# Kernel optimization log

Measured on AMD Instinct MI355X. Metric: run time of the kernel, lower is better.

The kernel has to match this reference:

```python
import jax, jax.numpy as jnp
import numpy as np

N_NODES = 50000
N_EDGES = 800000
F_IN = 128
HIDDEN = 32
HEADS = 4
F_OUT = 64
NEG_SLOPE = 0.2


def setup_inputs() -> dict:
    key = jax.random.key(0)
    ks = jax.random.split(key, 9)
    x = jax.random.normal(ks[0], (N_NODES, F_IN), dtype=jnp.float32)
    edge_index = jax.random.randint(ks[1], (2, N_EDGES), 0, N_NODES, dtype=jnp.int64)
    edge_weight = jax.random.uniform(ks[2], (N_EDGES,), dtype=jnp.float32)
    # GATConv parameters
    W = jax.random.normal(ks[3], (F_IN, HEADS * HIDDEN), dtype=jnp.float32) * (1.0 / np.sqrt(F_IN))
    a_src = jax.random.normal(ks[4], (HEADS, HIDDEN), dtype=jnp.float32) * 0.1
    a_dst = jax.random.normal(ks[5], (HEADS, HIDDEN), dtype=jnp.float32) * 0.1
    bias = jnp.zeros((HEADS * HIDDEN,), dtype=jnp.float32)
    # output linear
    W2 = jax.random.normal(ks[6], (HEADS * HIDDEN, F_OUT), dtype=jnp.float32) * (1.0 / np.sqrt(HEADS * HIDDEN))
    b2 = jnp.zeros((F_OUT,), dtype=jnp.float32)
    return {"x": x, "edge_index": edge_index, "edge_weight": edge_weight,
            "W": W, "a_src": a_src, "a_dst": a_dst, "bias": bias,
            "W2": W2, "b2": b2}


def reference(x, edge_index, edge_weight, W, a_src, a_dst, bias, W2, b2):
    src, dst = edge_index[0], edge_index[1]
    # linear transform per head: [N, H, C]
    h = (x @ W).reshape(-1, HEADS, HIDDEN)
    # per-node attention logits: [N, H]
    alpha_s = jnp.einsum('nhc,hc->nh', h, a_src)
    alpha_d = jnp.einsum('nhc,hc->nh', h, a_dst)
    # per-edge scores: [E, H]
    e = alpha_s[src] + alpha_d[dst]
    e = jnp.where(e >= 0, e, NEG_SLOPE * e)  # LeakyReLU(0.2)
    # segment softmax over destination neighborhoods
    m = jax.ops.segment_max(e, dst, num_segments=N_NODES)  # [N, H]
    ex = jnp.exp(e - m[dst])
    denom = jax.ops.segment_sum(ex, dst, num_segments=N_NODES)  # [N, H]
    alpha = ex / (denom[dst] + 1e-16)  # [E, H]
    # weighted scatter-add aggregation: [N, H, C]
    msgs = alpha[:, :, None] * h[src]
    out = jax.ops.segment_sum(msgs, dst, num_segments=N_NODES)
    out = out.reshape(-1, HEADS * HIDDEN) + bias
    out = jax.nn.elu(out)
    return out @ W2 + b2
```

## Files before the change

### kernel.cpp

```cpp
#include <hip/hip_runtime.h>

#define N_NODES 50000
#define N_EDGES 800000
#define F_IN 128
#define HH 128
#define HEADS 4
#define F_OUT 64
#define NEG_SLOPE 0.2f

#define NBIN ((N_NODES + 63) / 64)
#define XC 8
#define CAPXB 256
#define NCUR (NBIN * XC)
#define BINCAP (XC * CAPXB)

#define NODE_BLOCKS ((N_NODES + 31) / 32)
#define FILLB (N_EDGES / 256)
#define TOTAL_BLOCKS (NODE_BLOCKS + FILLB)
#define ZERO_BLOCKS ((NCUR + 255) / 256)

typedef __attribute__((ext_vector_type(8))) short short8v;
typedef __attribute__((ext_vector_type(4))) float float4v;

__device__ __forceinline__ unsigned short f2bf(float f) {
    unsigned int u = __float_as_uint(f);
    u = (u + 0x7FFFu + ((u >> 16) & 1u)) >> 16;
    return (unsigned short)u;
}
__device__ __forceinline__ float bf2f(unsigned short s) {
    return __uint_as_float((unsigned int)s << 16);
}

__global__ __launch_bounds__(256) void k_prep(
    const float* __restrict__ W, const float* __restrict__ a_src,
    const float* __restrict__ a_dst,
    unsigned short* __restrict__ Wf, unsigned short* __restrict__ Waf,
    int* __restrict__ cursor)
{
    const int b = blockIdx.x;
    const int t = threadIdx.x;

    if (b >= 9) {
        int i = (b - 9) * 256 + t;
        if (i < NCUR) cursor[i] = 0;
        return;
    }

    if (b < 8) {
        const int ks = b >> 1, nn = b & 1;
        const int w = t >> 6, lane = t & 63, l15 = lane & 15, l4 = lane >> 4;
        const int c  = w * 32 + nn * 16 + l15;
        const int kb = ks * 32 + l4 * 8;
        short8v frag;
        #pragma unroll
        for (int j = 0; j < 8; ++j)
            frag[j] = (short)f2bf(W[(size_t)(kb + j) * HH + c]);
        *(short8v*)&Wf[(size_t)((ks * 2 + nn) * 256 + t) * 8] = frag;
        return;
    }

    __shared__ float Wa[F_IN][8];
    #pragma unroll
    for (int i = 0; i < 4; ++i) {
        int idx = t * 4 + i;
        int k = idx >> 3, col = idx & 7;
        const float* av = (col < 4) ? a_src : a_dst;
        int hd = col & 3;
        float s = 0.f;
        #pragma unroll
        for (int cc = 0; cc < 32; ++cc)
            s = fmaf(W[(size_t)k * HH + hd * 32 + cc], av[hd * 32 + cc], s);
        Wa[k][col] = s;
    }
    __syncthreads();

    if (t < 64) {
        const int l15 = t & 15, l4 = t >> 4;
        #pragma unroll
        for (int ks = 0; ks < 4; ++ks) {
            short8v frag;
            #pragma unroll
            for (int j = 0; j < 8; ++j)
                frag[j] = (l15 < 8) ? (short)f2bf(Wa[ks * 32 + l4 * 8 + j][l15]) : (short)0;
            *(short8v*)&Waf[(size_t)(ks * 64 + t) * 8] = frag;
        }
    }
}

__global__ __launch_bounds__(256) void k_node_fill(
    const float* __restrict__ x,
    const unsigned short* __restrict__ Wf, const unsigned short* __restrict__ Waf,
    unsigned short* __restrict__ h_bf,
    float* __restrict__ as_out, float* __restrict__ ad_out,
    const int* __restrict__ ei, int* __restrict__ cursor, unsigned int* __restrict__ bins)
{
    __shared__ __align__(16) unsigned short xs[32][136];

    const int g = blockIdx.x;
    if (g % 3 != 0) {
        const int fidx = g - g / 3 - 1;
        if (fidx < FILLB) {
            const int vx = g & 7;
            int e = fidx * 256 + threadIdx.x;
            int S = ei[e];
            int D = ei[N_EDGES + e];
            int idx = (D >> 6) * XC + vx;
            int sl = atomicAdd(&cursor[idx], 1);
            if (sl < CAPXB)
                bins[(size_t)idx * CAPXB + sl] =
                    ((unsigned int)S << 6) | (unsigned int)(D & 63);
        }
        return;
    }

    const int tid  = threadIdx.x;
    const int base = (g / 3) * 32;

    for (int i = tid; i < 32 * 32; i += 256) {
        int r = i >> 5, c4 = i & 31;
        int n = base + r;
        float4 v = (n < N_NODES) ? *(const float4*)&x[(size_t)n * F_IN + c4 * 4]
                                 : make_float4(0.f, 0.f, 0.f, 0.f);
        ushort4 hv;
        hv.x = f2bf(v.x); hv.y = f2bf(v.y); hv.z = f2bf(v.z); hv.w = f2bf(v.w);
        *(ushort4*)&xs[r][c4 * 4] = hv;
    }
    __syncthreads();

    const int w    = tid >> 6;
    const int lane = tid & 63;
    const int l15  = lane & 15;
    const int l4   = lane >> 4;

    short8v bfrag[4][2], wafrag[4];
    #pragma unroll
    for (int ks = 0; ks < 4; ++ks) {
        bfrag[ks][0] = *(const short8v*)&Wf[(size_t)((ks * 2 + 0) * 256 + tid) * 8];
        bfrag[ks][1] = *(const short8v*)&Wf[(size_t)((ks * 2 + 1) * 256 + tid) * 8];
        wafrag[ks]   = *(const short8v*)&Waf[(size_t)(ks * 64 + lane) * 8];
    }

    float4v acc[2][2] = {};
    float4v accL[2] = {};
    #pragma unroll
    for (int ks = 0; ks < 4; ++ks) {
        short8v a0 = *(const short8v*)&xs[l15][ks * 32 + l4 * 8];
        short8v a1 = *(const short8v*)&xs[16 + l15][ks * 32 + l4 * 8];
        acc[0][0] = __builtin_amdgcn_mfma_f32_16x16x32_bf16(a0, bfrag[ks][0], acc[0][0], 0, 0, 0);
        acc[0][1] = __builtin_amdgcn_mfma_f32_16x16x32_bf16(a0, bfrag[ks][1], acc[0][1], 0, 0, 0);
        acc[1][0] = __builtin_amdgcn_mfma_f32_16x16x32_bf16(a1, bfrag[ks][0], acc[1][0], 0, 0, 0);
        acc[1][1] = __builtin_amdgcn_mfma_f32_16x16x32_bf16(a1, bfrag[ks][1], acc[1][1], 0, 0, 0);
        accL[0]   = __builtin_amdgcn_mfma_f32_16x16x32_bf16(a0, wafrag[ks], accL[0], 0, 0, 0);
        accL[1]   = __builtin_amdgcn_mfma_f32_16x16x32_bf16(a1, wafrag[ks], accL[1], 0, 0, 0);
    }

    if (w == 0 && l15 < 8) {
        #pragma unroll
        for (int m = 0; m < 2; ++m) {
            #pragma unroll
            for (int reg = 0; reg < 4; ++reg) {
                int node = base + m * 16 + l4 * 4 + reg;
                if (node >= N_NODES) continue;
                float lg = accL[m][reg];
                if (l15 < 4) as_out[node * HEADS + l15]       = lg;
                else         ad_out[node * HEADS + (l15 - 4)] = lg;
            }
        }
    }

    __syncthreads();
    #pragma unroll
    for (int m = 0; m < 2; ++m) {
        #pragma unroll
        for (int reg = 0; reg < 4; ++reg) {
            int r = m * 16 + l4 * 4 + reg;
            xs[r][w * 32 + l15]      = f2bf(acc[m][0][reg]);
            xs[r][w * 32 + 16 + l15] = f2bf(acc[m][1][reg]);
        }
    }
    __syncthreads();
    for (int i = tid; i < 32 * 16; i += 256) {
        int r = i >> 4, c8 = i & 15;
        int n = base + r;
        if (n < N_NODES)
            *(short8v*)&h_bf[(size_t)n * HH + c8 * 8] = *(const short8v*)&xs[r][c8 * 8];
    }
}

__global__ __launch_bounds__(256) void k_sort(
    const int* __restrict__ cursor, const unsigned int* __restrict__ bins,
    unsigned short* __restrict__ srcs_g, int2* __restrict__ offdeg)
{
    __shared__ unsigned int stg[BINCAP];
    __shared__ int lcnt[64], loff[64], lcur[64];
    __shared__ int scnt[XC], soff[XC], tot_s;

    const int bin = blockIdx.x;
    const int tid = threadIdx.x;

    if (tid < 64) { lcnt[tid] = 0; lcur[tid] = 0; }
    if (tid < XC) {
        int c = cursor[bin * XC + tid];
        scnt[tid] = c < CAPXB ? c : CAPXB;
    }
    __syncthreads();
    if (tid == 0) {
        int r = 0;
        #pragma unroll
        for (int j = 0; j < XC; ++j) { soff[j] = r; r += scnt[j]; }
        tot_s = r;
    }
    __syncthreads();
    #pragma unroll
    for (int sg = 0; sg < XC; ++sg) {
        int c = scnt[sg], o = soff[sg];
        const unsigned int* bp = &bins[(size_t)(bin * XC + sg) * CAPXB];
        for (int i = tid; i < c; i += 256) {
            unsigned int u = bp[i];
            stg[o + i] = u;
            atomicAdd(&lcnt[u & 63], 1);
        }
    }
    __syncthreads();
    if (tid == 0) {
        int r = 0;
        #pragma unroll
        for (int j = 0; j < 64; ++j) { loff[j] = r; r += lcnt[j]; }
    }
    __syncthreads();
    const int tot = tot_s;
    for (int i = tid; i < tot; i += 256) {
        unsigned int u = stg[i];
        int d = u & 63;
        int sl = loff[d] + atomicAdd(&lcur[d], 1);
        srcs_g[(size_t)bin * BINCAP + sl] = (unsigned short)(u >> 6);
    }
    if (tid < 64) {
        int n = bin * 64 + tid;
        if (n < N_NODES)
            offdeg[n] = make_int2(bin * BINCAP + loff[tid], lcnt[tid]);
    }
}

__global__ __launch_bounds__(256) void k_gather(
    const int2* __restrict__ offdeg, const unsigned short* __restrict__ srcs_g,
    const float* __restrict__ as_, const float* __restrict__ ad_,
    const unsigned short* __restrict__ h_bf, unsigned short* __restrict__ agg_bf)
{
    int gid = blockIdx.x * 256 + threadIdx.x;
    int n = gid >> 6;
    if (n >= N_NODES) return;
    const int lane = gid & 63;
    const int hd  = lane >> 4;
    const int e16 = lane & 15;

    const float advv = ad_[n * 4 + hd];
    const int2 od = offdeg[n];
    const unsigned short* brow = &srcs_g[od.x];
    const int deg = od.y;

    float accx = 0.f, accy = 0.f, sum = 0.f;

    for (int cb = 0; cb < deg; cb += 16) {
        int m = deg - cb; if (m > 16) m = 16;
        int s = 0; float exown = 0.f;
        if (e16 < m) {
            s = brow[cb + e16];
            float lg = as_[s * 4 + hd] + advv;
            lg = lg >= 0.f ? lg : NEG_SLOPE * lg;
            exown = __expf(lg);
        }

#define GAT_BODY(j)                                                            \
        {                                                                      \
            float al = __shfl(exown, (hd << 4) + (j));                         \
            int   sj = __shfl(s,     (hd << 4) + (j));                         \
            unsigned int hv = *(const unsigned int*)&h_bf[(size_t)sj * HH + lane * 2]; \
            sum += al;                                                         \
            accx = fmaf(al, __uint_as_float((hv & 0xFFFFu) << 16), accx);      \
            accy = fmaf(al, __uint_as_float(hv & 0xFFFF0000u), accy);          \
        }

        if (m == 16) {
            #pragma unroll
            for (int j = 0; j < 16; ++j) GAT_BODY(j)
        } else {
            for (int j = 0; j < m; ++j) GAT_BODY(j)
        }
#undef GAT_BODY
    }

    float inv = 1.f / (sum + 1e-16f);
    unsigned int packed = (unsigned int)f2bf(accx * inv)
                        | ((unsigned int)f2bf(accy * inv) << 16);
    *(unsigned int*)&agg_bf[(size_t)n * HH + lane * 2] = packed;
}

__global__ __launch_bounds__(256) void k_output(
    const unsigned short* __restrict__ agg_bf, const float* __restrict__ bias,
    const float* __restrict__ W2, const float* __restrict__ b2,
    float* __restrict__ out)
{
    __shared__ float eb[64][132];

    const int tid  = threadIdx.x;
    const int base = blockIdx.x * 64;

    for (int i = tid; i < 64 * 16; i += 256) {
        int r = i >> 4, c8 = i & 15;
        int n = base + r;
        float v[8];
        if (n < N_NODES) {
            ushort4 p0 = *(const ushort4*)&agg_bf[(size_t)n * HH + c8 * 8];
            ushort4 p1 = *(const ushort4*)&agg_bf[(size_t)n * HH + c8 * 8 + 4];
            v[0] = bf2f(p0.x); v[1] = bf2f(p0.y); v[2] = bf2f(p0.z); v[3] = bf2f(p0.w);
            v[4] = bf2f(p1.x); v[5] = bf2f(p1.y); v[6] = bf2f(p1.z); v[7] = bf2f(p1.w);
        } else {
            #pragma unroll
            for (int j = 0; j < 8; ++j) v[j] = 0.f;
        }
        #pragma unroll
        for (int j = 0; j < 8; ++j) {
            float t = v[j] + bias[c8 * 8 + j];
            eb[r][c8 * 8 + j] = t > 0.f ? t : __expf(t) - 1.f;
        }
    }
    __syncthreads();

    const int cg = tid & 15;
    const int q  = tid >> 4;

    float4 b2v = *(const float4*)&b2[cg * 4];
    float4 acc[4] = { b2v, b2v, b2v, b2v };
    for (int k4 = 0; k4 < 32; ++k4) {
        const float* wr = &W2[(k4 * 4) * F_OUT + cg * 4];
        float4 w0 = *(const float4*)(wr);
        float4 w1 = *(const float4*)(wr + F_OUT);
        float4 w2 = *(const float4*)(wr + 2 * F_OUT);
        float4 w3 = *(const float4*)(wr + 3 * F_OUT);
        #pragma unroll
        for (int j = 0; j < 4; ++j) {
            float4 xv = *(const float4*)&eb[q * 4 + j][k4 * 4];
            acc[j].x = fmaf(xv.x, w0.x, acc[j].x); acc[j].y = fmaf(xv.x, w0.y, acc[j].y);
            acc[j].z = fmaf(xv.x, w0.z, acc[j].z); acc[j].w = fmaf(xv.x, w0.w, acc[j].w);
            acc[j].x = fmaf(xv.y, w1.x, acc[j].x); acc[j].y = fmaf(xv.y, w1.y, acc[j].y);
            acc[j].z = fmaf(xv.y, w1.z, acc[j].z); acc[j].w = fmaf(xv.y, w1.w, acc[j].w);
            acc[j].x = fmaf(xv.z, w2.x, acc[j].x); acc[j].y = fmaf(xv.z, w2.y, acc[j].y);
            acc[j].z = fmaf(xv.z, w2.z, acc[j].z); acc[j].w = fmaf(xv.z, w2.w, acc[j].w);
            acc[j].x = fmaf(xv.w, w3.x, acc[j].x); acc[j].y = fmaf(xv.w, w3.y, acc[j].y);
            acc[j].z = fmaf(xv.w, w3.z, acc[j].z); acc[j].w = fmaf(xv.w, w3.w, acc[j].w);
        }
    }
    #pragma unroll
    for (int j = 0; j < 4; ++j) {
        int n = base + q * 4 + j;
        if (n < N_NODES)
            *(float4*)&out[(size_t)n * F_OUT + cg * 4] = acc[j];
    }
}

extern "C" void kernel_launch(void* const* d_in, const int* in_sizes, int n_in,
                              void* d_out, int out_size, void* d_ws, size_t ws_size,
                              hipStream_t stream)
{
    const float* x     = (const float*)d_in[0];
    const int*   ei    = (const int*)  d_in[1];
    const float* W     = (const float*)d_in[3];
    const float* a_src = (const float*)d_in[4];
    const float* a_dst = (const float*)d_in[5];
    const float* bias  = (const float*)d_in[6];
    const float* W2    = (const float*)d_in[7];
    const float* b2    = (const float*)d_in[8];
    float* out = (float*)d_out;

    char* ws = (char*)d_ws;
    unsigned short* Wf   = (unsigned short*)ws;
    unsigned short* Waf  = Wf + 8 * 256 * 8;
    unsigned short* h_bf = Waf + 4 * 64 * 8;
    float* as_   = (float*)(h_bf + (size_t)N_NODES * HH);
    float* ad_   = as_ + (size_t)N_NODES * HEADS;
    int*   cursor= (int*)(ad_ + (size_t)N_NODES * HEADS);
    unsigned int* bins = (unsigned int*)(cursor + 6400);
    unsigned short* srcs_g = (unsigned short*)(bins + (size_t)NBIN * BINCAP);
    int2*  offdeg = (int2*)(srcs_g + (size_t)NBIN * BINCAP);
    unsigned short* agg_bf = (unsigned short*)(offdeg + N_NODES + 2);

    k_prep<<<9 + ZERO_BLOCKS, 256, 0, stream>>>(W, a_src, a_dst, Wf, Waf, cursor);
    k_node_fill<<<TOTAL_BLOCKS, 256, 0, stream>>>(
        x, Wf, Waf, h_bf, as_, ad_, ei, cursor, bins);
    k_sort<<<NBIN, 256, 0, stream>>>(cursor, bins, srcs_g, offdeg);
    k_gather<<<(N_NODES * 64 + 255) / 256, 256, 0, stream>>>(
        offdeg, srcs_g, as_, ad_, h_bf, agg_bf);
    k_output<<<(N_NODES + 63) / 64, 256, 0, stream>>>(agg_bf, bias, W2, b2, out);
}
```

Measured before the change: 127.2 us.

## Split gather per head with head-major features and edge-parallel lane mapping

New measurement: 179.6 us. 1.41x slower.

```diff
diff --git a/kernel.cpp b/kernel.cpp
--- a/kernel.cpp
+++ b/kernel.cpp
@@ -29,6 +29,12 @@
 }
 __device__ __forceinline__ float bf2f(unsigned short s) {
     return __uint_as_float((unsigned int)s << 16);
+}
+__device__ __forceinline__ float bflo(unsigned int u) {
+    return __uint_as_float((u & 0xFFFFu) << 16);
+}
+__device__ __forceinline__ float bfhi(unsigned int u) {
+    return __uint_as_float(u & 0xFFFF0000u);
 }
 
 __global__ __launch_bounds__(256) void k_prep(
@@ -162,8 +168,8 @@
                 int node = base + m * 16 + l4 * 4 + reg;
                 if (node >= N_NODES) continue;
                 float lg = accL[m][reg];
-                if (l15 < 4) as_out[node * HEADS + l15]       = lg;
-                else         ad_out[node * HEADS + (l15 - 4)] = lg;
+                if (l15 < 4) as_out[l15 * N_NODES + node]       = lg;
+                else         ad_out[(l15 - 4) * N_NODES + node] = lg;
             }
         }
     }
@@ -182,8 +188,11 @@
     for (int i = tid; i < 32 * 16; i += 256) {
         int r = i >> 4, c8 = i & 15;
         int n = base + r;
-        if (n < N_NODES)
-            *(short8v*)&h_bf[(size_t)n * HH + c8 * 8] = *(const short8v*)&xs[r][c8 * 8];
+        if (n < N_NODES) {
+            int hd = c8 >> 2, o = (c8 & 3) * 8;
+            *(short8v*)&h_bf[((size_t)hd * N_NODES + n) * 32 + o] =
+                *(const short8v*)&xs[r][c8 * 8];
+        }
     }
 }
 
@@ -244,56 +253,61 @@
 
 __global__ __launch_bounds__(256) void k_gather(
     const int2* __restrict__ offdeg, const unsigned short* __restrict__ srcs_g,
-    const float* __restrict__ as_, const float* __restrict__ ad_,
-    const unsigned short* __restrict__ h_bf, unsigned short* __restrict__ agg_bf)
+    const float* __restrict__ as_h, const float* __restrict__ ad_h,
+    const unsigned short* __restrict__ h_h, unsigned short* __restrict__ agg_bf,
+    int hd)
 {
     int gid = blockIdx.x * 256 + threadIdx.x;
     int n = gid >> 6;
     if (n >= N_NODES) return;
     const int lane = gid & 63;
-    const int hd  = lane >> 4;
     const int e16 = lane & 15;
-
-    const float advv = ad_[n * 4 + hd];
+    const int grp = lane >> 4;
+
+    const float advv = ad_h[n];
     const int2 od = offdeg[n];
     const unsigned short* brow = &srcs_g[od.x];
     const int deg = od.y;
 
-    float accx = 0.f, accy = 0.f, sum = 0.f;
+    float a0 = 0.f, a1 = 0.f, a2 = 0.f, a3 = 0.f;
+    float a4 = 0.f, a5 = 0.f, a6 = 0.f, a7 = 0.f;
+    float sum = 0.f;
 
     for (int cb = 0; cb < deg; cb += 16) {
         int m = deg - cb; if (m > 16) m = 16;
-        int s = 0; float exown = 0.f;
+        int s = 0; float ex = 0.f;
         if (e16 < m) {
             s = brow[cb + e16];
-            float lg = as_[s * 4 + hd] + advv;
+            float lg = as_h[s] + advv;
             lg = lg >= 0.f ? lg : NEG_SLOPE * lg;
-            exown = __expf(lg);
-        }
-
-#define GAT_BODY(j)                                                            \
-        {                                                                      \
-            float al = __shfl(exown, (hd << 4) + (j));                         \
-            int   sj = __shfl(s,     (hd << 4) + (j));                         \
-            unsigned int hv = *(const unsigned int*)&h_bf[(size_t)sj * HH + lane * 2]; \
-            sum += al;                                                         \
-            accx = fmaf(al, __uint_as_float((hv & 0xFFFFu) << 16), accx);      \
-            accy = fmaf(al, __uint_as_float(hv & 0xFFFF0000u), accy);          \
-        }
-
-        if (m == 16) {
-            #pragma unroll
-            for (int j = 0; j < 16; ++j) GAT_BODY(j)
-        } else {
-            for (int j = 0; j < m; ++j) GAT_BODY(j)
-        }
-#undef GAT_BODY
-    }
-
-    float inv = 1.f / (sum + 1e-16f);
-    unsigned int packed = (unsigned int)f2bf(accx * inv)
-                        | ((unsigned int)f2bf(accy * inv) << 16);
-    *(unsigned int*)&agg_bf[(size_t)n * HH + lane * 2] = packed;
+            ex = __expf(lg);
+        }
+        sum += ex;
+        uint4 hv = *(const uint4*)&h_h[(size_t)s * 32 + grp * 8];
+        a0 = fmaf(ex, bflo(hv.x), a0); a1 = fmaf(ex, bfhi(hv.x), a1);
+        a2 = fmaf(ex, bflo(hv.y), a2); a3 = fmaf(ex, bfhi(hv.y), a3);
+        a4 = fmaf(ex, bflo(hv.z), a4); a5 = fmaf(ex, bfhi(hv.z), a5);
+        a6 = fmaf(ex, bflo(hv.w), a6); a7 = fmaf(ex, bfhi(hv.w), a7);
+    }
+
+    #pragma unroll
+    for (int off = 1; off < 16; off <<= 1) {
+        sum += __shfl_xor(sum, off);
+        a0 += __shfl_xor(a0, off); a1 += __shfl_xor(a1, off);
+        a2 += __shfl_xor(a2, off); a3 += __shfl_xor(a3, off);
+        a4 += __shfl_xor(a4, off); a5 += __shfl_xor(a5, off);
+        a6 += __shfl_xor(a6, off); a7 += __shfl_xor(a7, off);
+    }
+
+    if (e16 == 0) {
+        float inv = 1.f / (sum + 1e-16f);
+        uint4 o;
+        o.x = (unsigned int)f2bf(a0 * inv) | ((unsigned int)f2bf(a1 * inv) << 16);
+        o.y = (unsigned int)f2bf(a2 * inv) | ((unsigned int)f2bf(a3 * inv) << 16);
+        o.z = (unsigned int)f2bf(a4 * inv) | ((unsigned int)f2bf(a5 * inv) << 16);
+        o.w = (unsigned int)f2bf(a6 * inv) | ((unsigned int)f2bf(a7 * inv) << 16);
+        *(uint4*)&agg_bf[(size_t)n * HH + hd * 32 + grp * 8] = o;
+    }
 }
 
 __global__ __launch_bounds__(256) void k_output(
@@ -389,7 +403,11 @@
     k_node_fill<<<TOTAL_BLOCKS, 256, 0, stream>>>(
         x, Wf, Waf, h_bf, as_, ad_, ei, cursor, bins);
     k_sort<<<NBIN, 256, 0, stream>>>(cursor, bins, srcs_g, offdeg);
-    k_gather<<<(N_NODES * 64 + 255) / 256, 256, 0, stream>>>(
-        offdeg, srcs_g, as_, ad_, h_bf, agg_bf);
+    for (int hd = 0; hd < HEADS; ++hd) {
+        k_gather<<<(N_NODES * 64 + 255) / 256, 256, 0, stream>>>(
+            offdeg, srcs_g,
+            as_ + (size_t)hd * N_NODES, ad_ + (size_t)hd * N_NODES,
+            h_bf + (size_t)hd * N_NODES * 32, agg_bf, hd);
+    }
     k_output<<<(N_NODES + 63) / 64, 256, 0, stream>>>(agg_bf, bias, W2, b2, out);
 }
```
